# Performance work log

Hardware: AMD Instinct MI355X
Metric: run time of the kernel (lower is better)

## Reference

```python
import jax, jax.numpy as jnp
import numpy as np

INPUT_DIM = 1024
HIDDEN_DIM = 1024

def setup_inputs() -> dict:
    key = jax.random.key(0)
    ks = jax.random.split(key, 9)
    s_in = 1.0 / np.sqrt(INPUT_DIM)
    s_h = 1.0 / np.sqrt(HIDDEN_DIM)
    x = jax.random.normal(ks[0], (4, 2048, INPUT_DIM), dtype=jnp.float32)
    Wq = jax.random.uniform(ks[1], (INPUT_DIM, HIDDEN_DIM), jnp.float32, -s_in, s_in)
    bq = jax.random.uniform(ks[2], (HIDDEN_DIM,), jnp.float32, -s_in, s_in)
    Wk = jax.random.uniform(ks[3], (INPUT_DIM, HIDDEN_DIM), jnp.float32, -s_in, s_in)
    bk = jax.random.uniform(ks[4], (HIDDEN_DIM,), jnp.float32, -s_in, s_in)
    Wv = jax.random.uniform(ks[5], (INPUT_DIM, HIDDEN_DIM), jnp.float32, -s_in, s_in)
    bv = jax.random.uniform(ks[6], (HIDDEN_DIM,), jnp.float32, -s_in, s_in)
    Wo = jax.random.uniform(ks[7], (HIDDEN_DIM, INPUT_DIM), jnp.float32, -s_h, s_h)
    bo = jax.random.uniform(ks[8], (INPUT_DIM,), jnp.float32, -s_h, s_h)
    return {"x": x, "Wq": Wq, "bq": bq, "Wk": Wk, "bk": bk, "Wv": Wv, "bv": bv, "Wo": Wo, "bo": bo}

def reference(x, Wq, bq, Wk, bk, Wv, bv, Wo, bo):
    # x: [B, S, D_in]; scale uses x.shape[-1] (faithful to source, which divides by sqrt(input_dim))
    scale = 1.0 / jnp.sqrt(jnp.asarray(x.shape[-1], dtype=x.dtype))
    Q = jnp.einsum('bsd,dh->bsh', x, Wq) + bq
    K = jnp.einsum('bsd,dh->bsh', x, Wk) + bk
    V = jnp.einsum('bsd,dh->bsh', x, Wv) + bv
    scores = jnp.einsum('bqh,bkh->bqk', Q, K) * scale  # [B, S, S]
    attn = jax.nn.softmax(scores, axis=-1)
    ctx = jnp.einsum('bqk,bkh->bqh', attn, V)
    return jnp.einsum('bsh,hd->bsd', ctx, Wo) + bo
```

## Files before the change

### kernel.cpp

```cpp
#include <hip/hip_runtime.h>
#include <hip/hip_bf16.h>

typedef __attribute__((ext_vector_type(8))) short bf16x8;
typedef __attribute__((ext_vector_type(16))) float f32x16;

#define AS1 __attribute__((address_space(1)))
#define AS3 __attribute__((address_space(3)))

__device__ __forceinline__ unsigned short f2bf(float f) {
  unsigned u = __float_as_uint(f);
  u += 0x7fff + ((u >> 16) & 1);
  return (unsigned short)(u >> 16);
}

__device__ __forceinline__ void gload_lds16(const void* g, void* l) {
  __builtin_amdgcn_global_load_lds((const AS1 unsigned int*)g,
                                   (AS3 unsigned int*)l, 16, 0, 0);
}

template <typename OutT, bool BIAS, bool SPLIT, int NJ>
__global__ __launch_bounds__(256, (NJ == 4) ? 2 : 3) void gemm_bt(
    const unsigned short* __restrict__ A,
    const unsigned short* __restrict__ Bt,
    OutT* __restrict__ C,
    const float* __restrict__ bias,
    int Kd, int lda, int ldb, int ldc,
    long sA, long sB, long sC,
    float scale) {
  constexpr int BN    = NJ * 64;
  constexpr int ROWS  = 128 + BN;
  constexpr int SLOTS = ROWS / 16;
  __shared__ unsigned short lds[2][ROWS * 32];

  const int bz = blockIdx.z;
  A  += (size_t)bz * sA + (size_t)blockIdx.x * 128 * lda;
  Bt += (size_t)bz * sB + (size_t)blockIdx.y * BN * ldb;

  const int tid  = threadIdx.x;
  const int wave = tid >> 6;
  const int lane = tid & 63;
  const int wm   = (wave >> 1) * 64;
  const int wn   = (wave & 1) * (NJ * 32);
  const int l32  = lane & 31;
  const int half = lane >> 5;
  const int cg   = ((lane & 3) ^ ((lane >> 2) & 3) ^ (lane >> 4)) * 8;
  const int pswz = (l32 & 3) ^ ((l32 >> 2) & 3);

  auto stage = [&](int k0, int b) {
#pragma unroll
    for (int j = 0; j < SLOTS / 4; ++j) {
      const int s = wave + 4 * j;
      const int r = s * 16 + (lane >> 2);
      const unsigned short* src = (s < 8) ? (A + (size_t)r * lda)
                                          : (Bt + (size_t)(r - 128) * ldb);
      gload_lds16(src + k0 + cg, (char*)&lds[b][0] + s * 1024);
    }
  };

  f32x16 acc[2][NJ] = {};

  stage(0, 0);
  int cur = 0;
  for (int k0 = 0; k0 < Kd; k0 += 32) {
    __syncthreads();
    if (k0 + 32 < Kd) stage(k0 + 32, cur ^ 1);

    const unsigned short* base = &lds[cur][0];
    bf16x8 af[2][2], bfr[NJ][2];
#pragma unroll
    for (int t = 0; t < 2; ++t)
#pragma unroll
      for (int h = 0; h < 2; ++h) {
        const int p = ((2 * h + half) ^ pswz) * 8;
        af[t][h] = *(const bf16x8*)&base[(wm + t * 32 + l32) * 32 + p];
      }
#pragma unroll
    for (int u = 0; u < NJ; ++u)
#pragma unroll
      for (int h = 0; h < 2; ++h) {
        const int p = ((2 * h + half) ^ pswz) * 8;
        bfr[u][h] = *(const bf16x8*)&base[(128 + wn + u * 32 + l32) * 32 + p];
      }
#pragma unroll
    for (int t = 0; t < 2; ++t)
#pragma unroll
      for (int u = 0; u < NJ; ++u) {
        acc[t][u] = __builtin_amdgcn_mfma_f32_32x32x16_bf16(af[t][0], bfr[u][0], acc[t][u], 0, 0, 0);
        acc[t][u] = __builtin_amdgcn_mfma_f32_32x32x16_bf16(af[t][1], bfr[u][1], acc[t][u], 0, 0, 0);
      }
    cur ^= 1;
  }

  const int row0 = blockIdx.x * 128 + wm;
  const int colb = blockIdx.y * BN;
  int col0;
  if constexpr (SPLIT) {
    C += (size_t)(colb >> 10) * sC;
    col0 = (colb & 1023) + wn;
  } else {
    C += (size_t)bz * sC;
    col0 = colb + wn;
  }
#pragma unroll
  for (int t = 0; t < 2; ++t) {
#pragma unroll
    for (int u = 0; u < NJ; ++u) {
      const int col = col0 + u * 32 + l32;
      const float bv = BIAS ? bias[colb + wn + u * 32 + l32] : 0.0f;
#pragma unroll
      for (int r = 0; r < 16; ++r) {
        const int row = row0 + t * 32 + (r & 3) + 8 * (r >> 2) + 4 * half;
        const float v = acc[t][u][r] * scale + bv;
        if constexpr (sizeof(OutT) == 4)
          C[(size_t)row * ldc + col] = v;
        else
          C[(size_t)row * ldc + col] = (OutT)f2bf(v);
      }
    }
  }
}

__global__ void cvt_x(const float* __restrict__ in, unsigned short* __restrict__ out, int n4) {
  const int i = blockIdx.x * blockDim.x + threadIdx.x;
  if (i < n4) {
    const float4 v = ((const float4*)in)[i];
    uint2 o;
    o.x = (unsigned)f2bf(v.x) | ((unsigned)f2bf(v.y) << 16);
    o.y = (unsigned)f2bf(v.z) | ((unsigned)f2bf(v.w) << 16);
    ((uint2*)out)[i] = o;
  }
}

__global__ void cvtT_w4(const float* __restrict__ Wq, const float* __restrict__ Wk,
                        const float* __restrict__ Wv, const float* __restrict__ Wo,
                        unsigned short* __restrict__ Wqkvb, unsigned short* __restrict__ Wob) {
  __shared__ unsigned short tile[64][65];
  const int z = blockIdx.z;
  const float* in = (z == 0) ? Wq : (z == 1) ? Wk : (z == 2) ? Wv : Wo;
  unsigned short* out = (z == 3) ? Wob : Wqkvb + (size_t)z * 1024 * 1024;
  const int r0 = blockIdx.y * 64, c0 = blockIdx.x * 64;
  for (int i = threadIdx.y; i < 64; i += 4)
    tile[i][threadIdx.x] = f2bf(in[(size_t)(r0 + i) * 1024 + c0 + threadIdx.x]);
  __syncthreads();
  for (int i = threadIdx.y; i < 64; i += 4)
    out[(size_t)(c0 + i) * 1024 + r0 + threadIdx.x] = tile[threadIdx.x][i];
}

__global__ void concat_bias(const float* __restrict__ bq, const float* __restrict__ bk,
                            const float* __restrict__ bv, float* __restrict__ dst) {
  const int z = blockIdx.x;
  const float* src = (z == 0) ? bq : (z == 1) ? bk : bv;
  const int i = threadIdx.x;
  ((float4*)(dst + z * 1024))[i] = ((const float4*)src)[i];
}

__global__ void transpose_bf16(const unsigned short* __restrict__ in,
                               unsigned short* __restrict__ out, int rows, int cols) {
  __shared__ unsigned short tile[64][65];
  const int b = blockIdx.z;
  in  += (size_t)b * rows * cols;
  out += (size_t)b * rows * cols;
  const int r0 = blockIdx.y * 64, c0 = blockIdx.x * 64;
  for (int i = threadIdx.y; i < 64; i += 4)
    tile[i][threadIdx.x] = in[(size_t)(r0 + i) * cols + c0 + threadIdx.x];
  __syncthreads();
  for (int i = threadIdx.y; i < 64; i += 4)
    out[(size_t)(c0 + i) * rows + r0 + threadIdx.x] = tile[threadIdx.x][i];
}

__global__ __launch_bounds__(256) void softmax_inplace(float* __restrict__ scores) {
  float* p = scores + (size_t)blockIdx.x * 2048;
  const int t = threadIdx.x;
  float4 v0 = ((const float4*)p)[t * 2];
  float4 v1 = ((const float4*)p)[t * 2 + 1];

  float m = fmaxf(fmaxf(fmaxf(v0.x, v0.y), fmaxf(v0.z, v0.w)),
                  fmaxf(fmaxf(v1.x, v1.y), fmaxf(v1.z, v1.w)));
#pragma unroll
  for (int off = 32; off; off >>= 1) m = fmaxf(m, __shfl_xor(m, off, 64));

  __shared__ float red[4];
  __shared__ float bcast[2];
  const int wave = t >> 6, lane = t & 63;
  if (lane == 0) red[wave] = m;
  __syncthreads();
  if (t == 0) bcast[0] = fmaxf(fmaxf(red[0], red[1]), fmaxf(red[2], red[3]));
  __syncthreads();
  m = bcast[0];

  v0.x = __expf(v0.x - m); v0.y = __expf(v0.y - m);
  v0.z = __expf(v0.z - m); v0.w = __expf(v0.w - m);
  v1.x = __expf(v1.x - m); v1.y = __expf(v1.y - m);
  v1.z = __expf(v1.z - m); v1.w = __expf(v1.w - m);

  float s = v0.x + v0.y + v0.z + v0.w + v1.x + v1.y + v1.z + v1.w;
#pragma unroll
  for (int off = 32; off; off >>= 1) s += __shfl_xor(s, off, 64);
  if (lane == 0) red[wave] = s;
  __syncthreads();
  if (t == 0) bcast[1] = red[0] + red[1] + red[2] + red[3];
  __syncthreads();
  const float inv = 1.0f / bcast[1];

  uint4 ov;
  ov.x = (unsigned)f2bf(v0.x * inv) | ((unsigned)f2bf(v0.y * inv) << 16);
  ov.y = (unsigned)f2bf(v0.z * inv) | ((unsigned)f2bf(v0.w * inv) << 16);
  ov.z = (unsigned)f2bf(v1.x * inv) | ((unsigned)f2bf(v1.y * inv) << 16);
  ov.w = (unsigned)f2bf(v1.z * inv) | ((unsigned)f2bf(v1.w * inv) << 16);
  ((uint4*)p)[t] = ov;
}

extern "C" void kernel_launch(void* const* d_in, const int* in_sizes, int n_in,
                              void* d_out, int out_size, void* d_ws, size_t ws_size,
                              hipStream_t stream) {
  const float* x  = (const float*)d_in[0];
  const float* Wq = (const float*)d_in[1];
  const float* bq = (const float*)d_in[2];
  const float* Wk = (const float*)d_in[3];
  const float* bk = (const float*)d_in[4];
  const float* Wv = (const float*)d_in[5];
  const float* bv = (const float*)d_in[6];
  const float* Wo = (const float*)d_in[7];
  const float* bo = (const float*)d_in[8];
  float* out = (float*)d_out;

  char* ws = (char*)d_ws;
  size_t off = 0;
  auto alloc = [&](size_t bytes) { char* p = ws + off; off += (bytes + 255) & ~255UL; return p; };
  unsigned short* xb    = (unsigned short*)alloc(8192UL * 1024 * 2);
  unsigned short* Wqkvb = (unsigned short*)alloc(3072UL * 1024 * 2);
  unsigned short* Wob   = (unsigned short*)alloc(1024UL * 1024 * 2);
  float*          bqkv  = (float*)alloc(3072UL * 4);
  unsigned short* Qb    = (unsigned short*)alloc(8192UL * 1024 * 2);
  unsigned short* Kb    = (unsigned short*)alloc(8192UL * 1024 * 2);
  unsigned short* Vb    = (unsigned short*)alloc(8192UL * 1024 * 2);
  unsigned short* Vtb   = (unsigned short*)alloc(4UL * 1024 * 2048 * 2);
  unsigned short* ctxb  = (unsigned short*)alloc(8192UL * 1024 * 2);
  float*          sc    = (float*)alloc(4UL * 2048 * 2048 * 4);

  const dim3 blk(256);

  cvt_x<<<2097152 / 256, 256, 0, stream>>>(x, xb, 2097152);
  cvtT_w4<<<dim3(16, 16, 4), dim3(64, 4), 0, stream>>>(Wq, Wk, Wv, Wo, Wqkvb, Wob);
  concat_bias<<<3, 256, 0, stream>>>(bq, bk, bv, bqkv);

  gemm_bt<unsigned short, true, true, 4><<<dim3(64, 12, 1), blk, 0, stream>>>(
      xb, Wqkvb, Qb, bqkv, 1024, 1024, 1024, 1024, 0, 0, 8192L * 1024, 1.0f);

  transpose_bf16<<<dim3(16, 32, 4), dim3(64, 4), 0, stream>>>(Vb, Vtb, 2048, 1024);

  gemm_bt<float, false, false, 4><<<dim3(16, 8, 4), blk, 0, stream>>>(
      Qb, Kb, sc, nullptr, 1024, 1024, 1024, 2048,
      2048L * 1024, 2048L * 1024, 2048L * 2048, 0.03125f);

  softmax_inplace<<<8192, 256, 0, stream>>>(sc);

  gemm_bt<unsigned short, false, false, 2><<<dim3(16, 8, 4), blk, 0, stream>>>(
      (unsigned short*)sc, Vtb, ctxb, nullptr, 2048, 4096, 2048, 1024,
      2048L * 4096, 1024L * 2048, 2048L * 1024, 1.0f);

  gemm_bt<float, true, false, 2><<<dim3(64, 8, 1), blk, 0, stream>>>(
      ctxb, Wob, out, bo, 1024, 1024, 1024, 1024, 0, 0, 0, 1.0f);
}
```

Before: 317.6 us.

## Fuse V transpose into QKV GEMM epilogue and store scores in bf16

The QKV projection GEMM now writes V directly in transposed layout from its epilogue, which removes the separate transpose kernel and the intermediate V buffer; its N-tile changes from 256 to 192 columns. Attention scores are written as bf16 instead of fp32, so the score write and the softmax read carry half the bytes, and the softmax works on bf16 input. The transposed V stores are 8-byte strided writes, which may coalesce poorly. Rounding scores to bf16 before softmax adds precision loss.

```diff
diff --git a/kernel.cpp b/kernel.cpp
--- a/kernel.cpp
+++ b/kernel.cpp
@@ -3,6 +3,7 @@
 
 typedef __attribute__((ext_vector_type(8))) short bf16x8;
 typedef __attribute__((ext_vector_type(16))) float f32x16;
+typedef __attribute__((ext_vector_type(4))) unsigned short us4;
 
 #define AS1 __attribute__((address_space(1)))
 #define AS3 __attribute__((address_space(3)))
@@ -13,16 +14,21 @@
   return (unsigned short)(u >> 16);
 }
 
+__device__ __forceinline__ float bf2f(unsigned short h) {
+  return __uint_as_float((unsigned)h << 16);
+}
+
 __device__ __forceinline__ void gload_lds16(const void* g, void* l) {
   __builtin_amdgcn_global_load_lds((const AS1 unsigned int*)g,
                                    (AS3 unsigned int*)l, 16, 0, 0);
 }
 
-template <typename OutT, bool BIAS, bool SPLIT, int NJ>
-__global__ __launch_bounds__(256, (NJ == 4) ? 2 : 3) void gemm_bt(
+template <typename OutT, bool BIAS, int MODE, int NJ>
+__global__ __launch_bounds__(256, (NJ >= 3) ? 2 : 3) void gemm_bt(
     const unsigned short* __restrict__ A,
     const unsigned short* __restrict__ Bt,
     OutT* __restrict__ C,
+    unsigned short* __restrict__ Vt,
     const float* __restrict__ bias,
     int Kd, int lda, int ldb, int ldc,
     long sA, long sB, long sC,
@@ -93,28 +99,58 @@
 
   const int row0 = blockIdx.x * 128 + wm;
   const int colb = blockIdx.y * BN;
-  int col0;
-  if constexpr (SPLIT) {
-    C += (size_t)(colb >> 10) * sC;
-    col0 = (colb & 1023) + wn;
+
+  if constexpr (MODE == 1) {
+#pragma unroll
+    for (int t = 0; t < 2; ++t) {
+#pragma unroll
+      for (int u = 0; u < NJ; ++u) {
+        const int gcol  = colb + wn + u * 32;
+        const int piece = gcol >> 10;
+        const float bv  = BIAS ? bias[gcol + l32] : 0.0f;
+        if (piece < 2) {
+          OutT* dst = C + (size_t)piece * sC;
+          const int col = (gcol & 1023) + l32;
+#pragma unroll
+          for (int r = 0; r < 16; ++r) {
+            const int row = row0 + t * 32 + (r & 3) + 8 * (r >> 2) + 4 * half;
+            dst[(size_t)row * ldc + col] = (OutT)f2bf(acc[t][u][r] * scale + bv);
+          }
+        } else {
+          const int d = (gcol & 1023) + l32;
+          const int b = row0 >> 11;
+          const int sbase = (row0 & 2047) + t * 32 + 4 * half;
+#pragma unroll
+          for (int g = 0; g < 4; ++g) {
+            const int s0 = sbase + 8 * g;
+            us4 pk;
+            pk.x = f2bf(acc[t][u][4 * g + 0] * scale + bv);
+            pk.y = f2bf(acc[t][u][4 * g + 1] * scale + bv);
+            pk.z = f2bf(acc[t][u][4 * g + 2] * scale + bv);
+            pk.w = f2bf(acc[t][u][4 * g + 3] * scale + bv);
+            *(us4*)&Vt[((size_t)b << 21) + (size_t)d * 2048 + s0] = pk;
+          }
+        }
+      }
+    }
   } else {
     C += (size_t)bz * sC;
-    col0 = colb + wn;
-  }
-#pragma unroll
-  for (int t = 0; t < 2; ++t) {
-#pragma unroll
-    for (int u = 0; u < NJ; ++u) {
-      const int col = col0 + u * 32 + l32;
-      const float bv = BIAS ? bias[colb + wn + u * 32 + l32] : 0.0f;
-#pragma unroll
-      for (int r = 0; r < 16; ++r) {
-        const int row = row0 + t * 32 + (r & 3) + 8 * (r >> 2) + 4 * half;
-        const float v = acc[t][u][r] * scale + bv;
-        if constexpr (sizeof(OutT) == 4)
-          C[(size_t)row * ldc + col] = v;
-        else
-          C[(size_t)row * ldc + col] = (OutT)f2bf(v);
+    const int col0 = colb + wn;
+#pragma unroll
+    for (int t = 0; t < 2; ++t) {
+#pragma unroll
+      for (int u = 0; u < NJ; ++u) {
+        const int col = col0 + u * 32 + l32;
+        const float bv = BIAS ? bias[col0 + u * 32 + l32] : 0.0f;
+#pragma unroll
+        for (int r = 0; r < 16; ++r) {
+          const int row = row0 + t * 32 + (r & 3) + 8 * (r >> 2) + 4 * half;
+          const float v = acc[t][u][r] * scale + bv;
+          if constexpr (sizeof(OutT) == 4)
+            C[(size_t)row * ldc + col] = v;
+          else
+            C[(size_t)row * ldc + col] = (OutT)f2bf(v);
+        }
       }
     }
   }
@@ -154,28 +190,19 @@
   ((float4*)(dst + z * 1024))[i] = ((const float4*)src)[i];
 }
 
-__global__ void transpose_bf16(const unsigned short* __restrict__ in,
-                               unsigned short* __restrict__ out, int rows, int cols) {
-  __shared__ unsigned short tile[64][65];
-  const int b = blockIdx.z;
-  in  += (size_t)b * rows * cols;
-  out += (size_t)b * rows * cols;
-  const int r0 = blockIdx.y * 64, c0 = blockIdx.x * 64;
-  for (int i = threadIdx.y; i < 64; i += 4)
-    tile[i][threadIdx.x] = in[(size_t)(r0 + i) * cols + c0 + threadIdx.x];
-  __syncthreads();
-  for (int i = threadIdx.y; i < 64; i += 4)
-    out[(size_t)(c0 + i) * rows + r0 + threadIdx.x] = tile[threadIdx.x][i];
-}
-
-__global__ __launch_bounds__(256) void softmax_inplace(float* __restrict__ scores) {
-  float* p = scores + (size_t)blockIdx.x * 2048;
+__global__ __launch_bounds__(256) void softmax_bf16(unsigned short* __restrict__ scores) {
+  unsigned short* p = scores + (size_t)blockIdx.x * 2048;
   const int t = threadIdx.x;
-  float4 v0 = ((const float4*)p)[t * 2];
-  float4 v1 = ((const float4*)p)[t * 2 + 1];
-
-  float m = fmaxf(fmaxf(fmaxf(v0.x, v0.y), fmaxf(v0.z, v0.w)),
-                  fmaxf(fmaxf(v1.x, v1.y), fmaxf(v1.z, v1.w)));
+  uint4 raw = ((const uint4*)p)[t];
+  float v[8];
+  v[0] = __uint_as_float(raw.x << 16); v[1] = __uint_as_float(raw.x & 0xffff0000u);
+  v[2] = __uint_as_float(raw.y << 16); v[3] = __uint_as_float(raw.y & 0xffff0000u);
+  v[4] = __uint_as_float(raw.z << 16); v[5] = __uint_as_float(raw.z & 0xffff0000u);
+  v[6] = __uint_as_float(raw.w << 16); v[7] = __uint_as_float(raw.w & 0xffff0000u);
+
+  float m = v[0];
+#pragma unroll
+  for (int i = 1; i < 8; ++i) m = fmaxf(m, v[i]);
 #pragma unroll
   for (int off = 32; off; off >>= 1) m = fmaxf(m, __shfl_xor(m, off, 64));
 
@@ -188,12 +215,9 @@
   __syncthreads();
   m = bcast[0];
 
-  v0.x = __expf(v0.x - m); v0.y = __expf(v0.y - m);
-  v0.z = __expf(v0.z - m); v0.w = __expf(v0.w - m);
-  v1.x = __expf(v1.x - m); v1.y = __expf(v1.y - m);
-  v1.z = __expf(v1.z - m); v1.w = __expf(v1.w - m);
-
-  float s = v0.x + v0.y + v0.z + v0.w + v1.x + v1.y + v1.z + v1.w;
+  float s = 0.f;
+#pragma unroll
+  for (int i = 0; i < 8; ++i) { v[i] = __expf(v[i] - m); s += v[i]; }
 #pragma unroll
   for (int off = 32; off; off >>= 1) s += __shfl_xor(s, off, 64);
   if (lane == 0) red[wave] = s;
@@ -203,10 +227,10 @@
   const float inv = 1.0f / bcast[1];
 
   uint4 ov;
-  ov.x = (unsigned)f2bf(v0.x * inv) | ((unsigned)f2bf(v0.y * inv) << 16);
-  ov.y = (unsigned)f2bf(v0.z * inv) | ((unsigned)f2bf(v0.w * inv) << 16);
-  ov.z = (unsigned)f2bf(v1.x * inv) | ((unsigned)f2bf(v1.y * inv) << 16);
-  ov.w = (unsigned)f2bf(v1.z * inv) | ((unsigned)f2bf(v1.w * inv) << 16);
+  ov.x = (unsigned)f2bf(v[0] * inv) | ((unsigned)f2bf(v[1] * inv) << 16);
+  ov.y = (unsigned)f2bf(v[2] * inv) | ((unsigned)f2bf(v[3] * inv) << 16);
+  ov.z = (unsigned)f2bf(v[4] * inv) | ((unsigned)f2bf(v[5] * inv) << 16);
+  ov.w = (unsigned)f2bf(v[6] * inv) | ((unsigned)f2bf(v[7] * inv) << 16);
   ((uint4*)p)[t] = ov;
 }
 
@@ -233,10 +257,9 @@
   float*          bqkv  = (float*)alloc(3072UL * 4);
   unsigned short* Qb    = (unsigned short*)alloc(8192UL * 1024 * 2);
   unsigned short* Kb    = (unsigned short*)alloc(8192UL * 1024 * 2);
-  unsigned short* Vb    = (unsigned short*)alloc(8192UL * 1024 * 2);
   unsigned short* Vtb   = (unsigned short*)alloc(4UL * 1024 * 2048 * 2);
+  unsigned short* attn  = (unsigned short*)alloc(8192UL * 2048 * 2);
   unsigned short* ctxb  = (unsigned short*)alloc(8192UL * 1024 * 2);
-  float*          sc    = (float*)alloc(4UL * 2048 * 2048 * 4);
 
   const dim3 blk(256);
 
@@ -244,21 +267,19 @@
   cvtT_w4<<<dim3(16, 16, 4), dim3(64, 4), 0, stream>>>(Wq, Wk, Wv, Wo, Wqkvb, Wob);
   concat_bias<<<3, 256, 0, stream>>>(bq, bk, bv, bqkv);
 
-  gemm_bt<unsigned short, true, true, 4><<<dim3(64, 12, 1), blk, 0, stream>>>(
-      xb, Wqkvb, Qb, bqkv, 1024, 1024, 1024, 1024, 0, 0, 8192L * 1024, 1.0f);
-
-  transpose_bf16<<<dim3(16, 32, 4), dim3(64, 4), 0, stream>>>(Vb, Vtb, 2048, 1024);
-
-  gemm_bt<float, false, false, 4><<<dim3(16, 8, 4), blk, 0, stream>>>(
-      Qb, Kb, sc, nullptr, 1024, 1024, 1024, 2048,
+  gemm_bt<unsigned short, true, 1, 3><<<dim3(64, 16, 1), blk, 0, stream>>>(
+      xb, Wqkvb, Qb, Vtb, bqkv, 1024, 1024, 1024, 1024, 0, 0, 8192L * 1024, 1.0f);
+
+  gemm_bt<unsigned short, false, 0, 4><<<dim3(16, 8, 4), blk, 0, stream>>>(
+      Qb, Kb, attn, nullptr, nullptr, 1024, 1024, 1024, 2048,
       2048L * 1024, 2048L * 1024, 2048L * 2048, 0.03125f);
 
-  softmax_inplace<<<8192, 256, 0, stream>>>(sc);
-
-  gemm_bt<unsigned short, false, false, 2><<<dim3(16, 8, 4), blk, 0, stream>>>(
-      (unsigned short*)sc, Vtb, ctxb, nullptr, 2048, 4096, 2048, 1024,
-      2048L * 4096, 1024L * 2048, 2048L * 1024, 1.0f);
-
-  gemm_bt<float, true, false, 2><<<dim3(64, 8, 1), blk, 0, stream>>>(
-      ctxb, Wob, out, bo, 1024, 1024, 1024, 1024, 0, 0, 0, 1.0f);
-}
+  softmax_bf16<<<8192, 256, 0, stream>>>(attn);
+
+  gemm_bt<unsigned short, false, 0, 2><<<dim3(16, 8, 4), blk, 0, stream>>>(
+      attn, Vtb, ctxb, nullptr, nullptr, 2048, 2048, 2048, 1024,
+      2048L * 2048, 1024L * 2048, 2048L * 1024, 1.0f);
+
+  gemm_bt<float, true, 0, 2><<<dim3(64, 8, 1), blk, 0, stream>>>(
+      ctxb, Wob, out, nullptr, bo, 1024, 1024, 1024, 1024, 0, 0, 0, 1.0f);
+}
```

After: 300.2 us. 5.5% less time.
